# Performance work log

Hardware: AMD Instinct MI355X
Metric: run time of the kernel (lower is better)

Reference implementation:

```python
import jax, jax.numpy as jnp
import numpy as np

B, T, D, U = 32, 4096, 512, 256

def setup_inputs() -> dict:
    key = jax.random.key(0)
    ks = jax.random.split(key, 5)
    s = 1.0 / np.sqrt(D)
    return {
        "values": jax.random.normal(ks[0], (B, T, D), dtype=jnp.float32),
        "query": jax.random.normal(ks[1], (B, D), dtype=jnp.float32),
        "W1": jax.random.normal(ks[2], (D, U), dtype=jnp.float32) * s,
        "b1": jnp.zeros((U,), dtype=jnp.float32),
        "W2": jax.random.normal(ks[3], (D, U), dtype=jnp.float32) * s,
        "b2": jnp.zeros((U,), dtype=jnp.float32),
        "V": jax.random.normal(ks[4], (U, 1), dtype=jnp.float32) * (1.0 / np.sqrt(U)),
        "bV": jnp.zeros((1,), dtype=jnp.float32),
    }

def reference(values, query, W1, b1, W2, b2, V, bV):
    # values: [B,T,D], query: [B,D]
    h_vals = jnp.einsum('btd,du->btu', values, W1) + b1          # [B,T,U]
    h_query = (query @ W2 + b2)[:, None, :]                       # [B,1,U]
    score = jnp.einsum('btu,uo->bto', jnp.tanh(h_vals + h_query), V) + bV  # [B,T,1]
    attention_weights = jax.nn.softmax(score, axis=1)             # [B,T,1]
    context_vector = jnp.sum(attention_weights * values, axis=1)  # [B,D]
    return context_vector, attention_weights
```

## Files before the change

kernel.cpp:

```cpp
#include <hip/hip_runtime.h>
#include <math.h>
#include <stdint.h>

#define BB 32
#define TT 4096
#define DD 512
#define UU 256

#define KC 32
#define NKC (DD/KC)
#define NST (NKC/2)
#define LDA2 72
#define NTILE (TT/64)

typedef __attribute__((ext_vector_type(8))) short short8;
typedef __attribute__((ext_vector_type(8))) unsigned short ushort8;
typedef __attribute__((ext_vector_type(4))) float floatx4;

__device__ __forceinline__ unsigned short bf16_rne(float x) {
  union { float f; uint32_t u; } v; v.f = x;
  uint32_t r = v.u + 0x7FFFu + ((v.u >> 16) & 1u);
  return (unsigned short)(r >> 16);
}
__device__ __forceinline__ unsigned int cvt_pk_bf16(float a, float b) {
  unsigned int r;
  asm("v_cvt_pk_bf16_f32 %0, %1, %2" : "=v"(r) : "v"(a), "v"(b));
  return r;
}
__device__ __forceinline__ float tanh_fast(float x) {
  float e = __expf(2.0f * x);
  return 1.0f - 2.0f * __builtin_amdgcn_rcpf(e + 1.0f);
}

#define BAR_LDS()                                     \
  do {                                                \
    asm volatile("s_waitcnt lgkmcnt(0)" ::: "memory");\
    __builtin_amdgcn_s_barrier();                     \
  } while (0)

__global__ __launch_bounds__(256) void setup_kernel(
    const float* __restrict__ W1, unsigned short* __restrict__ w1t,
    const float* __restrict__ query, const float* __restrict__ W2,
    const float* __restrict__ b2, const float* __restrict__ b1,
    float* __restrict__ hq) {
  __shared__ float qs[DD];
  if (blockIdx.x < NKC) {
    const int kc = blockIdx.x;
    const int u = threadIdx.x;
    __attribute__((aligned(16))) unsigned short row[KC];
#pragma unroll
    for (int kk = 0; kk < KC; ++kk)
      row[kk] = bf16_rne(W1[(kc * KC + kk) * UU + u]);
    unsigned short* dst = w1t + ((size_t)kc * UU + u) * KC;
#pragma unroll
    for (int i = 0; i < 4; ++i) ((uint4*)dst)[i] = *(const uint4*)&row[i * 8];
  } else {
    const int b = blockIdx.x - NKC;
    const int u = threadIdx.x;
    for (int d = threadIdx.x; d < DD; d += 256) qs[d] = query[b * DD + d];
    __syncthreads();
    float a0 = 0.f, a1 = 0.f, a2 = 0.f, a3 = 0.f;
#pragma unroll 4
    for (int d = 0; d < DD; d += 4) {
      a0 += qs[d + 0] * W2[(d + 0) * UU + u];
      a1 += qs[d + 1] * W2[(d + 1) * UU + u];
      a2 += qs[d + 2] * W2[(d + 2) * UU + u];
      a3 += qs[d + 3] * W2[(d + 3) * UU + u];
    }
    hq[b * UU + u] = (a0 + a1) + (a2 + a3) + b2[u] + b1[u];
  }
}

__global__ __launch_bounds__(256, 2) void score_kernel(
    const float* __restrict__ values, const unsigned short* __restrict__ w1t,
    const float* __restrict__ hq, const float* __restrict__ V,
    const float* __restrict__ bV, float* __restrict__ scores,
    float* __restrict__ pml, float* __restrict__ pctx) {
  const int b = blockIdx.y;
  const int blk = blockIdx.x;
  const int t0 = blk * 64;
  const int tid = threadIdx.x;
  const int wave = tid >> 6;
  const int lane = tid & 63;
  const int c = lane & 15;
  const int q = lane >> 4;

  __shared__ unsigned short As[2][64 * LDA2];
  __shared__ float redW[4][64];
  __shared__ float warr[64];

  floatx4 acc[4][4];
#pragma unroll
  for (int ti = 0; ti < 4; ++ti)
#pragma unroll
    for (int ui = 0; ui < 4; ++ui) acc[ti][ui] = (floatx4){0.f, 0.f, 0.f, 0.f};

  const int ar = tid >> 2;
  const int aseg = tid & 3;
  const float* asrc =
      values + ((size_t)b * TT + t0 + ar) * DD + aseg * 8;

  const unsigned short* bbase = w1t + ((size_t)(wave * 64 + c)) * KC + q * 8;

  float4 aq[2][4];
  short8 bfr[2][8];

#pragma unroll
  for (int j = 0; j < 2; ++j) {
    aq[0][2 * j + 0] = *(const float4*)(asrc + j * KC);
    aq[0][2 * j + 1] = *(const float4*)(asrc + j * KC + 4);
    aq[1][2 * j + 0] = *(const float4*)(asrc + (2 + j) * KC);
    aq[1][2 * j + 1] = *(const float4*)(asrc + (2 + j) * KC + 4);
  }
#pragma unroll
  for (int j = 0; j < 2; ++j)
#pragma unroll
    for (int ui = 0; ui < 4; ++ui)
      bfr[0][j * 4 + ui] =
          *(const short8*)(bbase + ((size_t)(j * UU) + ui * 16) * KC);

#pragma unroll
  for (int s = 0; s < NST; ++s) {
    const int buf = s & 1;
    {
      uint4 w0, w1;
      w0.x = cvt_pk_bf16(aq[buf][0].x, aq[buf][0].y);
      w0.y = cvt_pk_bf16(aq[buf][0].z, aq[buf][0].w);
      w0.z = cvt_pk_bf16(aq[buf][1].x, aq[buf][1].y);
      w0.w = cvt_pk_bf16(aq[buf][1].z, aq[buf][1].w);
      w1.x = cvt_pk_bf16(aq[buf][2].x, aq[buf][2].y);
      w1.y = cvt_pk_bf16(aq[buf][2].z, aq[buf][2].w);
      w1.z = cvt_pk_bf16(aq[buf][3].x, aq[buf][3].y);
      w1.w = cvt_pk_bf16(aq[buf][3].z, aq[buf][3].w);
      *(uint4*)&As[buf][ar * LDA2 + aseg * 8] = w0;
      *(uint4*)&As[buf][ar * LDA2 + 32 + aseg * 8] = w1;
    }
    if (s + 2 < NST) {
#pragma unroll
      for (int j = 0; j < 2; ++j) {
        aq[buf][2 * j + 0] = *(const float4*)(asrc + (2 * (s + 2) + j) * KC);
        aq[buf][2 * j + 1] =
            *(const float4*)(asrc + (2 * (s + 2) + j) * KC + 4);
      }
    }
    BAR_LDS();
    if (s + 1 < NST) {
#pragma unroll
      for (int j = 0; j < 2; ++j)
#pragma unroll
        for (int ui = 0; ui < 4; ++ui)
          bfr[buf ^ 1][j * 4 + ui] = *(const short8*)(
              bbase + ((size_t)(2 * (s + 1) + j) * UU + ui * 16) * KC);
    }
    {
      short8 afr[4];
#pragma unroll
      for (int ti = 0; ti < 4; ++ti)
        afr[ti] = *(const short8*)&As[buf][(ti * 16 + c) * LDA2 + q * 8];
      __builtin_amdgcn_s_setprio(1);
#pragma unroll
      for (int ti = 0; ti < 4; ++ti)
#pragma unroll
        for (int ui = 0; ui < 4; ++ui)
          acc[ti][ui] = __builtin_amdgcn_mfma_f32_16x16x32_bf16(
              afr[ti], bfr[buf][ui], acc[ti][ui], 0, 0, 0);
      __builtin_amdgcn_s_setprio(0);
    }
    {
      short8 afr[4];
#pragma unroll
      for (int ti = 0; ti < 4; ++ti)
        afr[ti] = *(const short8*)&As[buf][(ti * 16 + c) * LDA2 + 32 + q * 8];
      __builtin_amdgcn_s_setprio(1);
#pragma unroll
      for (int ti = 0; ti < 4; ++ti)
#pragma unroll
        for (int ui = 0; ui < 4; ++ui)
          acc[ti][ui] = __builtin_amdgcn_mfma_f32_16x16x32_bf16(
              afr[ti], bfr[buf][4 + ui], acc[ti][ui], 0, 0, 0);
      __builtin_amdgcn_s_setprio(0);
    }
  }

  float hqv[4], vv[4];
#pragma unroll
  for (int ui = 0; ui < 4; ++ui) {
    const int u = wave * 64 + ui * 16 + c;
    hqv[ui] = hq[b * UU + u];
    vv[ui] = V[u];
  }
#pragma unroll
  for (int ti = 0; ti < 4; ++ti)
#pragma unroll
    for (int r = 0; r < 4; ++r) {
      float e = 0.0f;
#pragma unroll
      for (int ui = 0; ui < 4; ++ui)
        e += tanh_fast(acc[ti][ui][r] + hqv[ui]) * vv[ui];
      e += __shfl_xor(e, 1, 64);
      e += __shfl_xor(e, 2, 64);
      e += __shfl_xor(e, 4, 64);
      e += __shfl_xor(e, 8, 64);
      if (c == 0) redW[wave][ti * 16 + q * 4 + r] = e;
    }
  __syncthreads();
  if (tid < 64) {
    const float s =
        bV[0] + redW[0][tid] + redW[1][tid] + redW[2][tid] + redW[3][tid];
    scores[b * TT + t0 + tid] = s;
    redW[0][tid] = s;
  }
  __syncthreads();
  float mb = -1e30f;
#pragma unroll 8
  for (int t = 0; t < 64; ++t) mb = fmaxf(mb, redW[0][t]);
  if (tid < 64) warr[tid] = __expf(redW[0][tid] - mb);
  __syncthreads();
  float lb = 0.0f;
#pragma unroll 8
  for (int t = 0; t < 64; ++t) lb += warr[t];

  const float2* vp = (const float2*)(values + ((size_t)b * TT + t0) * DD);
  float2 c2 = {0.f, 0.f};
#pragma unroll 4
  for (int t = 0; t < 64; ++t) {
    const float w = warr[t];
    const float2 v = vp[(size_t)t * (DD / 2) + tid];
    c2.x += w * v.x;
    c2.y += w * v.y;
  }
  *(float2*)&pctx[((size_t)b * NTILE + blk) * DD + 2 * tid] = c2;
  if (tid == 0) {
    pml[(b * NTILE + blk) * 2 + 0] = mb;
    pml[(b * NTILE + blk) * 2 + 1] = lb;
  }
}

__global__ __launch_bounds__(256) void combine_kernel(
    const float* __restrict__ pml, const float* __restrict__ pctx,
    const float* __restrict__ scores, float* __restrict__ out) {
  const int b = blockIdx.x;
  const int tid = threadIdx.x;
  __shared__ float mls[2 * NTILE];
  __shared__ float cs[NTILE];
  if (tid < 2 * NTILE) mls[tid] = pml[b * 2 * NTILE + tid];
  __syncthreads();
  float m = -1e30f;
#pragma unroll 8
  for (int i = 0; i < NTILE; ++i) m = fmaxf(m, mls[2 * i]);
  if (tid < NTILE) cs[tid] = __expf(mls[2 * tid] - m);
  __syncthreads();
  float l = 0.0f;
#pragma unroll 8
  for (int i = 0; i < NTILE; ++i) l += cs[i] * mls[2 * i + 1];
  const float linv = 1.0f / l;

  const float2* pp = (const float2*)(pctx + (size_t)b * NTILE * DD);
  float2 acc = {0.f, 0.f};
#pragma unroll 4
  for (int i = 0; i < NTILE; ++i) {
    const float cw = cs[i];
    const float2 p = pp[(size_t)i * (DD / 2) + tid];
    acc.x += cw * p.x;
    acc.y += cw * p.y;
  }
  out[b * DD + 2 * tid + 0] = acc.x * linv;
  out[b * DD + 2 * tid + 1] = acc.y * linv;

  float* wout = out + BB * DD + (size_t)b * TT;
  const float* srow = scores + (size_t)b * TT;
#pragma unroll
  for (int i = 0; i < TT / 256; ++i) {
    const int t = i * 256 + tid;
    wout[t] = __expf(srow[t] - m) * linv;
  }
}

extern "C" void kernel_launch(void* const* d_in, const int* in_sizes, int n_in,
                              void* d_out, int out_size, void* d_ws, size_t ws_size,
                              hipStream_t stream) {
  const float* values = (const float*)d_in[0];
  const float* query  = (const float*)d_in[1];
  const float* W1     = (const float*)d_in[2];
  const float* b1     = (const float*)d_in[3];
  const float* W2     = (const float*)d_in[4];
  const float* b2     = (const float*)d_in[5];
  const float* V      = (const float*)d_in[6];
  const float* bV     = (const float*)d_in[7];
  float* out = (float*)d_out;

  float* ws = (float*)d_ws;
  float* hq     = ws;
  float* scores = ws + BB * UU;
  float* pml    = scores + BB * TT;
  float* pctx   = pml + BB * NTILE * 2;
  unsigned short* w1t = (unsigned short*)(pctx + (size_t)BB * NTILE * DD);

  setup_kernel<<<NKC + BB, 256, 0, stream>>>(W1, w1t, query, W2, b2, b1, hq);
  score_kernel<<<dim3(NTILE, BB), 256, 0, stream>>>(
      values, w1t, hq, V, bV, scores, pml, pctx);
  combine_kernel<<<BB, 256, 0, stream>>>(pml, pctx, scores, out);
}
```

Baseline: 434.7 us.

## Fuse combine into score kernel via last-block ticket; deepen A prefetch

The separate combine kernel is removed. Each score block now increments a per-batch atomic counter, and the last block to finish for each batch does the softmax renormalisation and context reduction, which saves one launch and the tail gap between kernels. The A-operand register prefetch is deepened from 2 to 3 stages, and the B fragments are reloaded right after each half-step's MFMAs, cutting the B buffers to half size. This raises VGPR pressure for the A buffers and adds a serialized tail in the last block of each batch.

After: 912.1 us. +109.8%, slower.

```diff
diff --git a/kernel.cpp b/kernel.cpp
--- a/kernel.cpp
+++ b/kernel.cpp
@@ -42,11 +42,12 @@
     const float* __restrict__ W1, unsigned short* __restrict__ w1t,
     const float* __restrict__ query, const float* __restrict__ W2,
     const float* __restrict__ b2, const float* __restrict__ b1,
-    float* __restrict__ hq) {
+    float* __restrict__ hq, unsigned int* __restrict__ cnt) {
   __shared__ float qs[DD];
   if (blockIdx.x < NKC) {
     const int kc = blockIdx.x;
     const int u = threadIdx.x;
+    if (blockIdx.x == 0 && threadIdx.x < BB) cnt[threadIdx.x] = 0u;
     __attribute__((aligned(16))) unsigned short row[KC];
 #pragma unroll
     for (int kk = 0; kk < KC; ++kk)
@@ -75,7 +76,8 @@
     const float* __restrict__ values, const unsigned short* __restrict__ w1t,
     const float* __restrict__ hq, const float* __restrict__ V,
     const float* __restrict__ bV, float* __restrict__ scores,
-    float* __restrict__ pml, float* __restrict__ pctx) {
+    float* __restrict__ pml, float* __restrict__ pctx,
+    unsigned int* __restrict__ cnt, float* __restrict__ out) {
   const int b = blockIdx.y;
   const int blk = blockIdx.x;
   const int t0 = blk * 64;
@@ -88,6 +90,7 @@
   __shared__ unsigned short As[2][64 * LDA2];
   __shared__ float redW[4][64];
   __shared__ float warr[64];
+  __shared__ unsigned int ticket_s;
 
   floatx4 acc[4][4];
 #pragma unroll
@@ -102,56 +105,49 @@
 
   const unsigned short* bbase = w1t + ((size_t)(wave * 64 + c)) * KC + q * 8;
 
-  float4 aq[2][4];
-  short8 bfr[2][8];
-
-#pragma unroll
-  for (int j = 0; j < 2; ++j) {
-    aq[0][2 * j + 0] = *(const float4*)(asrc + j * KC);
-    aq[0][2 * j + 1] = *(const float4*)(asrc + j * KC + 4);
-    aq[1][2 * j + 0] = *(const float4*)(asrc + (2 + j) * KC);
-    aq[1][2 * j + 1] = *(const float4*)(asrc + (2 + j) * KC + 4);
-  }
+  float4 aq[3][4];
+  short8 bfr[2][4];
+
+#pragma unroll
+  for (int s0 = 0; s0 < 3; ++s0)
+#pragma unroll
+    for (int j = 0; j < 2; ++j) {
+      aq[s0][2 * j + 0] = *(const float4*)(asrc + (2 * s0 + j) * KC);
+      aq[s0][2 * j + 1] = *(const float4*)(asrc + (2 * s0 + j) * KC + 4);
+    }
 #pragma unroll
   for (int j = 0; j < 2; ++j)
 #pragma unroll
     for (int ui = 0; ui < 4; ++ui)
-      bfr[0][j * 4 + ui] =
+      bfr[j][ui] =
           *(const short8*)(bbase + ((size_t)(j * UU) + ui * 16) * KC);
 
 #pragma unroll
   for (int s = 0; s < NST; ++s) {
+    const int sl = s % 3;
     const int buf = s & 1;
     {
       uint4 w0, w1;
-      w0.x = cvt_pk_bf16(aq[buf][0].x, aq[buf][0].y);
-      w0.y = cvt_pk_bf16(aq[buf][0].z, aq[buf][0].w);
-      w0.z = cvt_pk_bf16(aq[buf][1].x, aq[buf][1].y);
-      w0.w = cvt_pk_bf16(aq[buf][1].z, aq[buf][1].w);
-      w1.x = cvt_pk_bf16(aq[buf][2].x, aq[buf][2].y);
-      w1.y = cvt_pk_bf16(aq[buf][2].z, aq[buf][2].w);
-      w1.z = cvt_pk_bf16(aq[buf][3].x, aq[buf][3].y);
-      w1.w = cvt_pk_bf16(aq[buf][3].z, aq[buf][3].w);
+      w0.x = cvt_pk_bf16(aq[sl][0].x, aq[sl][0].y);
+      w0.y = cvt_pk_bf16(aq[sl][0].z, aq[sl][0].w);
+      w0.z = cvt_pk_bf16(aq[sl][1].x, aq[sl][1].y);
+      w0.w = cvt_pk_bf16(aq[sl][1].z, aq[sl][1].w);
+      w1.x = cvt_pk_bf16(aq[sl][2].x, aq[sl][2].y);
+      w1.y = cvt_pk_bf16(aq[sl][2].z, aq[sl][2].w);
+      w1.z = cvt_pk_bf16(aq[sl][3].x, aq[sl][3].y);
+      w1.w = cvt_pk_bf16(aq[sl][3].z, aq[sl][3].w);
       *(uint4*)&As[buf][ar * LDA2 + aseg * 8] = w0;
       *(uint4*)&As[buf][ar * LDA2 + 32 + aseg * 8] = w1;
     }
-    if (s + 2 < NST) {
+    if (s + 3 < NST) {
 #pragma unroll
       for (int j = 0; j < 2; ++j) {
-        aq[buf][2 * j + 0] = *(const float4*)(asrc + (2 * (s + 2) + j) * KC);
-        aq[buf][2 * j + 1] =
-            *(const float4*)(asrc + (2 * (s + 2) + j) * KC + 4);
+        aq[sl][2 * j + 0] = *(const float4*)(asrc + (2 * (s + 3) + j) * KC);
+        aq[sl][2 * j + 1] =
+            *(const float4*)(asrc + (2 * (s + 3) + j) * KC + 4);
       }
     }
     BAR_LDS();
-    if (s + 1 < NST) {
-#pragma unroll
-      for (int j = 0; j < 2; ++j)
-#pragma unroll
-        for (int ui = 0; ui < 4; ++ui)
-          bfr[buf ^ 1][j * 4 + ui] = *(const short8*)(
-              bbase + ((size_t)(2 * (s + 1) + j) * UU + ui * 16) * KC);
-    }
     {
       short8 afr[4];
 #pragma unroll
@@ -163,8 +159,14 @@
 #pragma unroll
         for (int ui = 0; ui < 4; ++ui)
           acc[ti][ui] = __builtin_amdgcn_mfma_f32_16x16x32_bf16(
-              afr[ti], bfr[buf][ui], acc[ti][ui], 0, 0, 0);
+              afr[ti], bfr[0][ui], acc[ti][ui], 0, 0, 0);
       __builtin_amdgcn_s_setprio(0);
+    }
+    if (2 * s + 2 < NKC) {
+#pragma unroll
+      for (int ui = 0; ui < 4; ++ui)
+        bfr[0][ui] = *(const short8*)(
+            bbase + ((size_t)(2 * s + 2) * UU + ui * 16) * KC);
     }
     {
       short8 afr[4];
@@ -177,8 +179,14 @@
 #pragma unroll
         for (int ui = 0; ui < 4; ++ui)
           acc[ti][ui] = __builtin_amdgcn_mfma_f32_16x16x32_bf16(
-              afr[ti], bfr[buf][4 + ui], acc[ti][ui], 0, 0, 0);
+              afr[ti], bfr[1][ui], acc[ti][ui], 0, 0, 0);
       __builtin_amdgcn_s_setprio(0);
+    }
+    if (2 * s + 3 < NKC) {
+#pragma unroll
+      for (int ui = 0; ui < 4; ++ui)
+        bfr[1][ui] = *(const short8*)(
+            bbase + ((size_t)(2 * s + 3) * UU + ui * 16) * KC);
     }
   }
 
@@ -234,45 +242,44 @@
     pml[(b * NTILE + blk) * 2 + 0] = mb;
     pml[(b * NTILE + blk) * 2 + 1] = lb;
   }
-}
-
-__global__ __launch_bounds__(256) void combine_kernel(
-    const float* __restrict__ pml, const float* __restrict__ pctx,
-    const float* __restrict__ scores, float* __restrict__ out) {
-  const int b = blockIdx.x;
-  const int tid = threadIdx.x;
-  __shared__ float mls[2 * NTILE];
-  __shared__ float cs[NTILE];
-  if (tid < 2 * NTILE) mls[tid] = pml[b * 2 * NTILE + tid];
+
+  __threadfence();
+  if (tid == 0) ticket_s = atomicAdd(&cnt[b], 1u);
   __syncthreads();
-  float m = -1e30f;
+  if (ticket_s == NTILE - 1) {
+    __threadfence();
+    float* mls = &redW[0][0];
+    if (tid < 2 * NTILE) mls[tid] = pml[b * 2 * NTILE + tid];
+    __syncthreads();
+    float m = -1e30f;
 #pragma unroll 8
-  for (int i = 0; i < NTILE; ++i) m = fmaxf(m, mls[2 * i]);
-  if (tid < NTILE) cs[tid] = __expf(mls[2 * tid] - m);
-  __syncthreads();
-  float l = 0.0f;
+    for (int i = 0; i < NTILE; ++i) m = fmaxf(m, mls[2 * i]);
+    if (tid < NTILE) warr[tid] = __expf(mls[2 * tid] - m);
+    __syncthreads();
+    float l = 0.0f;
 #pragma unroll 8
-  for (int i = 0; i < NTILE; ++i) l += cs[i] * mls[2 * i + 1];
-  const float linv = 1.0f / l;
-
-  const float2* pp = (const float2*)(pctx + (size_t)b * NTILE * DD);
-  float2 acc = {0.f, 0.f};
+    for (int i = 0; i < NTILE; ++i) l += warr[i] * mls[2 * i + 1];
+    const float linv = 1.0f / l;
+
+    const float2* pp = (const float2*)(pctx + (size_t)b * NTILE * DD);
+    float2 a2 = {0.f, 0.f};
 #pragma unroll 4
-  for (int i = 0; i < NTILE; ++i) {
-    const float cw = cs[i];
-    const float2 p = pp[(size_t)i * (DD / 2) + tid];
-    acc.x += cw * p.x;
-    acc.y += cw * p.y;
-  }
-  out[b * DD + 2 * tid + 0] = acc.x * linv;
-  out[b * DD + 2 * tid + 1] = acc.y * linv;
-
-  float* wout = out + BB * DD + (size_t)b * TT;
-  const float* srow = scores + (size_t)b * TT;
-#pragma unroll
-  for (int i = 0; i < TT / 256; ++i) {
-    const int t = i * 256 + tid;
-    wout[t] = __expf(srow[t] - m) * linv;
+    for (int i = 0; i < NTILE; ++i) {
+      const float cw = warr[i];
+      const float2 p = pp[(size_t)i * (DD / 2) + tid];
+      a2.x += cw * p.x;
+      a2.y += cw * p.y;
+    }
+    out[b * DD + 2 * tid + 0] = a2.x * linv;
+    out[b * DD + 2 * tid + 1] = a2.y * linv;
+
+    float* wout = out + BB * DD + (size_t)b * TT;
+    const float* srow = scores + (size_t)b * TT;
+#pragma unroll
+    for (int i = 0; i < TT / 256; ++i) {
+      const int t = i * 256 + tid;
+      wout[t] = __expf(srow[t] - m) * linv;
+    }
   }
 }
 
@@ -293,11 +300,11 @@
   float* hq     = ws;
   float* scores = ws + BB * UU;
   float* pml    = scores + BB * TT;
-  float* pctx   = pml + BB * NTILE * 2;
+  unsigned int* cnt = (unsigned int*)(pml + BB * NTILE * 2);
+  float* pctx   = (float*)(cnt + BB);
   unsigned short* w1t = (unsigned short*)(pctx + (size_t)BB * NTILE * DD);
 
-  setup_kernel<<<NKC + BB, 256, 0, stream>>>(W1, w1t, query, W2, b2, b1, hq);
+  setup_kernel<<<NKC + BB, 256, 0, stream>>>(W1, w1t, query, W2, b2, b1, hq, cnt);
   score_kernel<<<dim3(NTILE, BB), 256, 0, stream>>>(
-      values, w1t, hq, V, bV, scores, pml, pctx);
-  combine_kernel<<<BB, 256, 0, stream>>>(pml, pctx, scores, out);
-}
+      values, w1t, hq, V, bV, scores, pml, pctx, cnt, out);
+}
```
